# Kernel optimization log

Hardware: AMD Instinct MI355X
Metric: run time of the kernel (lower is better)

## Reference

```python
import jax, jax.numpy as jnp
import numpy as np

B, F_DIM, FH, FW = 2, 2048, 64, 128
C, H, W = 19, 512, 1024


def resize_bilinear_ac(x, h, w):
    # align_corners=True bilinear resize of (B, C, H, W) -> (B, C, h, w)
    Bx, Cx, Hx, Wx = x.shape
    ys = jnp.linspace(0.0, Hx - 1.0, h)
    xs = jnp.linspace(0.0, Wx - 1.0, w)
    y0 = jnp.floor(ys).astype(jnp.int32)
    y1 = jnp.minimum(y0 + 1, Hx - 1)
    wy = (ys - y0).astype(x.dtype)
    x0 = jnp.floor(xs).astype(jnp.int32)
    x1 = jnp.minimum(x0 + 1, Wx - 1)
    wx = (xs - x0).astype(x.dtype)
    r = x[:, :, y0, :] * (1 - wy)[None, None, :, None] + x[:, :, y1, :] * wy[None, None, :, None]
    return r[:, :, :, x0] * (1 - wx) + r[:, :, :, x1] * wx


def setup_inputs() -> dict:
    key = jax.random.key(0)
    k1, k2, k3, k4 = jax.random.split(key, 4)
    return {
        "source_feat": jax.random.normal(k1, (B, F_DIM, FH, FW), dtype=jnp.float32),
        "source_softmax": jax.random.uniform(k2, (B, C, H, W), dtype=jnp.float32),
        "target_feat": jax.random.normal(k3, (B, F_DIM, FH, FW), dtype=jnp.float32),
        "target_softmax": jax.random.uniform(k4, (B, C, H, W), dtype=jnp.float32),
        "norm_order": 2,
    }


def _process(feat, softmax):
    # feat: (B, F, h, w) -> (B*h*w, F); labels from bilinear-downsampled softmax argmax
    h, w = feat.shape[2], feat.shape[3]
    f2 = feat.transpose(0, 2, 3, 1).reshape(-1, feat.shape[1])
    sm_dws = resize_bilinear_ac(softmax, h, w)
    labels = jnp.argmax(sm_dws, axis=1).reshape(-1)
    return f2, labels


def _forward(source_feat, source_softmax, target_feat, target_softmax, p):
    num_class = source_softmax.shape[1]
    fdim = source_feat.shape[1]
    sf, sl = _process(source_feat, source_softmax)
    tf, tl = _process(target_feat, target_softmax)

    # mixed centroids: per-class mean over concatenated source+target pixels
    sum_s = jax.ops.segment_sum(sf, sl, num_segments=num_class)
    cnt_s = jax.ops.segment_sum(jnp.ones(sf.shape[0], sf.dtype), sl, num_segments=num_class)
    sum_t = jax.ops.segment_sum(tf, tl, num_segments=num_class)
    cnt_t = jax.ops.segment_sum(jnp.ones(tf.shape[0], tf.dtype), tl, num_segments=num_class)
    cnt = cnt_s + cnt_t
    seen = cnt > 0
    centroids = (sum_s + sum_t) / jnp.maximum(cnt, 1.0)[:, None]  # (C, F)

    inv_p = 1.0 / p

    def f_dist(f2, lab, cnt_d):
        # torch: sum_i norm(centroid_i - feat_i, p) / (n_i * F) over classes with n_i>0, / count
        dp = jnp.sum(jnp.abs(f2 - centroids[lab]) ** p, axis=1)  # (N,)
        ssq = jax.ops.segment_sum(dp, lab, num_segments=num_class)  # (C,)
        valid = cnt_d > 0
        ssq_safe = jnp.where(valid, ssq, 1.0)
        per = ssq_safe ** inv_p / (jnp.maximum(cnt_d, 1.0) * fdim)
        return jnp.sum(jnp.where(valid, per, 0.0)) / jnp.sum(valid).astype(f2.dtype)

    f_dist_source = f_dist(sf, sl, cnt_s)
    f_dist_target = f_dist(tf, tl, cnt_t)

    # intra-domain centroid-to-centroid distance over seen classes
    n_seen = jnp.sum(seen).astype(centroids.dtype)
    diffp = jnp.sum(jnp.abs(centroids[:, None, :] - centroids[None, :, :]) ** p, axis=-1)  # (C, C)
    pair_mask = seen[:, None] & seen[None, :] & (~jnp.eye(num_class, dtype=bool))
    row = jnp.sum(jnp.where(pair_mask, diffp, 0.0), axis=1)
    row_safe = jnp.where(seen, row, 1.0)
    per_i = row_safe ** inv_p / ((n_seen - 1.0) * fdim)
    c_dist = jnp.sum(jnp.where(seen, per_i, 0.0)) / n_seen

    return jnp.stack([c_dist, f_dist_source, f_dist_target])


def reference(source_feat, source_softmax, target_feat, target_softmax, norm_order):
    return _forward(source_feat, source_softmax, target_feat, target_softmax, norm_order)
```

## Files before the change

### kernel.cpp

```cpp
#include <hip/hip_runtime.h>
#include <hip/hip_bf16.h>

#define BB 2
#define FDIM 2048
#define FH 64
#define FW 128
#define NPIX (FH*FW)
#define NC 19
#define SH 512
#define SW 1024

#define KS 4
#define PXS (NPIX/KS)

#define OFF_GCNT  0
#define OFF_SQP   38912
#define OFF_SUMP  194560
#define OFF_LAB   2684928
#define OFF_CENT  2717696
#define OFF_DOTSP 2873344
#define OFF_PQP   2875168
#define OFF_CNTF  2876384
#define OFF_ROW   2876536

typedef __attribute__((ext_vector_type(8))) short short8v;
typedef __attribute__((ext_vector_type(4))) float f32x4;
typedef __attribute__((ext_vector_type(4))) float f4v;

__device__ inline short f32_to_bf16_bits(float x) {
  __hip_bfloat16 h = __float2bfloat16(x);
  return *reinterpret_cast<short*>(&h);
}
__device__ inline float bf16_bits_to_f32(short s) {
  unsigned u = ((unsigned)s & 0xFFFFu) << 16;
  return __uint_as_float(u);
}

__global__ __launch_bounds__(256) void labels_kernel(
    const float* __restrict__ sm_s, const float* __restrict__ sm_t,
    unsigned char* __restrict__ labels, unsigned int* __restrict__ gcnt) {
  __shared__ unsigned int lcnt[NC];
  int tid = threadIdx.x;
  if (tid < NC) lcnt[tid] = 0u;
  __syncthreads();

  int g = blockIdx.x * 256 + tid;
  int pixid = g >> 2;
  int sub = g & 3;
  int dom = pixid >> 14;
  int rem = pixid & 16383;
  int b   = rem >> 13;
  int pix = rem & (NPIX - 1);
  int oy  = pix >> 7;
  int ox  = pix & (FW - 1);

  const float* sm = dom ? sm_t : sm_s;

  const float step_y = 511.0f / 63.0f;
  const float step_x = 1023.0f / 127.0f;
  float fy = __fmul_rn((float)oy, step_y);
  float fx = __fmul_rn((float)ox, step_x);
  int y0 = (int)floorf(fy); int y1 = min(y0 + 1, SH - 1);
  int x0 = (int)floorf(fx); int x1 = min(x0 + 1, SW - 1);
  float wy = __fsub_rn(fy, (float)y0);
  float wx = __fsub_rn(fx, (float)x0);
  float omwy = __fsub_rn(1.0f, wy);
  float omwx = __fsub_rn(1.0f, wx);

  const float* base = sm + (size_t)b * (NC * SH * SW);
  float best = -1.0f; int bestc = 127;
  for (int c = sub; c < NC; c += 4) {
    const float* p = base + (size_t)c * (SH * SW);
    float v00 = p[y0 * SW + x0];
    float v01 = p[y0 * SW + x1];
    float v10 = p[y1 * SW + x0];
    float v11 = p[y1 * SW + x1];
    float r0  = __fadd_rn(__fmul_rn(v00, omwy), __fmul_rn(v10, wy));
    float r1  = __fadd_rn(__fmul_rn(v01, omwy), __fmul_rn(v11, wy));
    float val = __fadd_rn(__fmul_rn(r0, omwx), __fmul_rn(r1, wx));
    if (val > best) { best = val; bestc = c; }
  }
#pragma unroll
  for (int off = 1; off <= 2; off <<= 1) {
    float ov = __shfl_xor(best, off, 64);
    int   oc = __shfl_xor(bestc, off, 64);
    if (ov > best || (ov == best && oc < bestc)) { best = ov; bestc = oc; }
  }
  if (sub == 0) {
    labels[pixid] = (unsigned char)bestc;
    atomicAdd(&lcnt[bestc], 1u);
  }
  __syncthreads();
  if (tid < NC) gcnt[blockIdx.x * NC + tid] = lcnt[tid];
}

__global__ __launch_bounds__(256, 8) void segsum_kernel(
    const float* __restrict__ feat_s, const float* __restrict__ feat_t,
    const unsigned char* __restrict__ labels,
    float* __restrict__ sump, float* __restrict__ sq_p) {
  __shared__ unsigned short Abuf[4][2][16][64];

  int tid = threadIdx.x;
  int wv = tid >> 6, l = tid & 63;
  int m16 = l & 15, grp = l >> 4;
  int lrow = l >> 4;
  int lpx  = (l & 15) * 4;

  int low = blockIdx.x & 255;
  int hi  = blockIdx.x >> 8;
  int d = low >> 7, strip = low & 127;
  int b = hi & 1, ks = hi >> 1;

  const float* feat = d ? feat_t : feat_s;
  int px0 = ks * PXS + wv * 512;
  const float* fbase = feat + ((size_t)(b * FDIM + strip * 16)) * NPIX + px0;
  const unsigned char* labp = labels + (d * 2 + b) * NPIX + px0;

  unsigned short (*mybuf)[16][64] = Abuf[wv];

  f32x4 accS0 = {0.f,0.f,0.f,0.f}, accS1 = {0.f,0.f,0.f,0.f};
  f32x4 accQ0 = {0.f,0.f,0.f,0.f}, accQ1 = {0.f,0.f,0.f,0.f};

  f4v ld0[4], ld1[4];

#define LOADW(REG, W)                                                         \
  _Pragma("unroll") for (int r = 0; r < 4; ++r)                               \
    REG[r] = __builtin_nontemporal_load(                                      \
        (const f4v*)(fbase + (size_t)(r * 4 + lrow) * NPIX + (W) * 64 + lpx));

#define WRITEW(REG, CUR)                                                      \
  _Pragma("unroll") for (int r = 0; r < 4; ++r) {                             \
    int row = r * 4 + lrow;                                                   \
    unsigned u0 = ((unsigned)(unsigned short)f32_to_bf16_bits(REG[r].x)) |    \
                  (((unsigned)(unsigned short)f32_to_bf16_bits(REG[r].y)) << 16);\
    unsigned u1 = ((unsigned)(unsigned short)f32_to_bf16_bits(REG[r].z)) |    \
                  (((unsigned)(unsigned short)f32_to_bf16_bits(REG[r].w)) << 16);\
    int wbyte = (row * 128 + lpx * 2) ^ ((row & 7) << 4);                     \
    *(uint2*)((char*)&mybuf[CUR][0][0] + wbyte) = make_uint2(u0, u1);         \
  }

#define COMPW(W, CUR)                                                         \
  _Pragma("unroll") for (int t = 0; t < 2; ++t) {                             \
    int rbyte = (m16 * 128 + t * 64 + grp * 16) ^ ((m16 & 7) << 4);           \
    short8v a = *(const short8v*)((const char*)&mybuf[CUR][0][0] + rbyte);    \
    short8v a2;                                                               \
    _Pragma("unroll") for (int j = 0; j < 8; ++j) {                           \
      float x = bf16_bits_to_f32(a[j]);                                       \
      a2[j] = f32_to_bf16_bits(x * x);                                        \
    }                                                                         \
    uint2 lw = *(const uint2*)(labp + (W) * 64 + t * 32 + grp * 8);           \
    short8v b0, b1;                                                           \
    _Pragma("unroll") for (int j = 0; j < 8; ++j) {                           \
      unsigned lab = ((j < 4 ? lw.x : lw.y) >> ((j & 3) * 8)) & 0xFFu;        \
      b0[j] = (lab == (unsigned)m16)        ? (short)0x3F80 : (short)0;       \
      b1[j] = (lab == (unsigned)(m16 + 16)) ? (short)0x3F80 : (short)0;       \
    }                                                                         \
    accS0 = __builtin_amdgcn_mfma_f32_16x16x32_bf16(a,  b0, accS0, 0, 0, 0);  \
    accS1 = __builtin_amdgcn_mfma_f32_16x16x32_bf16(a,  b1, accS1, 0, 0, 0);  \
    accQ0 = __builtin_amdgcn_mfma_f32_16x16x32_bf16(a2, b0, accQ0, 0, 0, 0);  \
    accQ1 = __builtin_amdgcn_mfma_f32_16x16x32_bf16(a2, b1, accQ1, 0, 0, 0);  \
  }

  LOADW(ld0, 0);
  WRITEW(ld0, 0);
  LOADW(ld0, 1);

#pragma unroll
  for (int w = 0; w < 8; w += 2) {
    if (w + 2 < 8) { LOADW(ld1, w + 2); }
    COMPW(w, 0);
    if (w + 1 < 8) { WRITEW(ld0, 1); }
    if (w + 3 < 8) { LOADW(ld0, w + 3); }
    COMPW(w + 1, 1);
    if (w + 2 < 8) { WRITEW(ld1, 0); }
  }
#undef LOADW
#undef WRITEW
#undef COMPW

  __syncthreads();
  float* Sred = (float*)&Abuf[0][0][0][0];
  float* Qred = Sred + 4 * 19 * 16;

  int c0 = l & 15, frb = (l >> 4) * 4;
  *(f32x4*)&Sred[(wv * 19 + c0) * 16 + frb] = accS0;
  if (c0 < 3) *(f32x4*)&Sred[(wv * 19 + 16 + c0) * 16 + frb] = accS1;

  float q0 = accQ0[0] + accQ0[1] + accQ0[2] + accQ0[3];
  float q1 = accQ1[0] + accQ1[1] + accQ1[2] + accQ1[3];
  q0 += __shfl_xor(q0, 16, 64); q0 += __shfl_xor(q0, 32, 64);
  q1 += __shfl_xor(q1, 16, 64); q1 += __shfl_xor(q1, 32, 64);
  if (l < 16) Qred[wv * 19 + l] = q0;
  if (l < 3)  Qred[wv * 19 + 16 + l] = q1;
  __syncthreads();

  float* myslice = sump + ((size_t)(hi * 2 + d) * NC) * FDIM + strip * 16;
  for (int t = tid; t < NC * 16; t += 256) {
    int c = t >> 4, fr = t & 15;
    float sv = Sred[(0 * 19 + c) * 16 + fr] + Sred[(1 * 19 + c) * 16 + fr] +
               Sred[(2 * 19 + c) * 16 + fr] + Sred[(3 * 19 + c) * 16 + fr];
    myslice[(size_t)c * FDIM + fr] = sv;
  }
  if (tid < NC) {
    float qv = Qred[tid] + Qred[19 + tid] + Qred[38 + tid] + Qred[57 + tid];
    sq_p[(size_t)((hi * 2 + d) * 128 + strip) * NC + tid] = qv;
  }
}

__device__ inline float block_reduce(float v, float* red, int tid) {
  red[tid] = v; __syncthreads();
  for (int s = 128; s > 0; s >>= 1) {
    if (tid < s) red[tid] += red[tid + s];
    __syncthreads();
  }
  float r = red[0];
  __syncthreads();
  return r;
}

__global__ __launch_bounds__(256) void centroid_kernel(
    const float* __restrict__ sump, const float* __restrict__ sq_p,
    const unsigned int* __restrict__ gcnt,
    float* __restrict__ cent, float* __restrict__ dotsp,
    float* __restrict__ pqp, float* __restrict__ cntf) {
  __shared__ float red[256];
  int bid = blockIdx.x;
  int c = bid % NC, j = bid / NC;
  int tid = threadIdx.x;

  float cs = block_reduce((float)gcnt[tid * NC + c], red, tid);
  float ct = block_reduce((float)gcnt[(256 + tid) * NC + c], red, tid);
  if (tid == 0 && j == 0) { cntf[c] = cs; cntf[NC + c] = ct; }
  float denom = fmaxf(cs + ct, 1.0f);

  int f = j * 256 + tid;
  float ssv = 0.f, stv = 0.f;
#pragma unroll
  for (int hi = 0; hi < 8; ++hi) {
    ssv += sump[((size_t)(hi * 2 + 0) * NC + c) * FDIM + f];
    stv += sump[((size_t)(hi * 2 + 1) * NC + c) * FDIM + f];
  }
  float cf = (ssv + stv) / denom;
  cent[(size_t)c * FDIM + f] = cf;

  float rds = block_reduce(cf * ssv, red, tid);
  float rdt = block_reduce(cf * stv, red, tid);
  float rcc = block_reduce(cf * cf, red, tid);

  int slice = tid >> 4, strip = j * 16 + (tid & 15);
  float v = sq_p[(size_t)(slice * 128 + strip) * NC + c];
  float qs = block_reduce((slice & 1) == 0 ? v : 0.f, red, tid);
  float qt = block_reduce((slice & 1) == 1 ? v : 0.f, red, tid);

  if (tid == 0) {
    dotsp[(j * NC + c) * 3 + 0] = rds;
    dotsp[(j * NC + c) * 3 + 1] = rdt;
    dotsp[(j * NC + c) * 3 + 2] = rcc;
    pqp[(j * NC + c) * 2 + 0] = qs;
    pqp[(j * NC + c) * 2 + 1] = qt;
  }
}

__global__ __launch_bounds__(256) void pair_kernel(
    const float* __restrict__ cent, const float* __restrict__ cntf,
    float* __restrict__ row) {
  __shared__ float red[256];
  int i = blockIdx.x;
  int tid = threadIdx.x;
  bool seen_i = (cntf[i] + cntf[NC + i]) > 0.f;
  float acc = 0.f;
  if (seen_i) {
    for (int j = 0; j < NC; ++j) {
      if (j == i) continue;
      if ((cntf[j] + cntf[NC + j]) <= 0.f) continue;
      for (int f = tid; f < FDIM; f += 256) {
        float dd = cent[(size_t)i * FDIM + f] - cent[(size_t)j * FDIM + f];
        acc += dd * dd;
      }
    }
  }
  float r = block_reduce(acc, red, tid);
  if (tid == 0) row[i] = r;
}

__global__ void final_kernel(
    const float* __restrict__ cntf, const float* __restrict__ dotsp,
    const float* __restrict__ pqp, const float* __restrict__ row,
    float* __restrict__ out) {
  int l = threadIdx.x;
  const float fdim = (float)FDIM;
  bool isC = l < NC;
  int c = isC ? l : 0;

  float cs = 0.f, ct = 0.f, qs = 0.f, qt = 0.f;
  float d_s = 0.f, d_t = 0.f, cc = 0.f, rw = 0.f;
  if (isC) {
    cs = cntf[c]; ct = cntf[NC + c];
#pragma unroll
    for (int j = 0; j < 8; ++j) {
      qs  += pqp[(j * NC + c) * 2 + 0];
      qt  += pqp[(j * NC + c) * 2 + 1];
      d_s += dotsp[(j * NC + c) * 3 + 0];
      d_t += dotsp[(j * NC + c) * 3 + 1];
      cc  += dotsp[(j * NC + c) * 3 + 2];
    }
    rw = row[c];
  }
  bool seen = isC && (cs + ct > 0.f);
  float nseenf = (float)__popcll(__ballot(seen));
  float nvs    = (float)__popcll(__ballot(isC && cs > 0.f));
  float nvt    = (float)__popcll(__ballot(isC && ct > 0.f));

  float fs = 0.f, ft = 0.f, cd = 0.f;
  if (isC && cs > 0.f) {
    float ssq = fmaxf(qs - 2.0f * d_s + cs * cc, 0.f);
    fs = sqrtf(ssq) / (cs * fdim);
  }
  if (isC && ct > 0.f) {
    float ssq = fmaxf(qt - 2.0f * d_t + ct * cc, 0.f);
    ft = sqrtf(ssq) / (ct * fdim);
  }
  if (seen) cd = sqrtf(rw) / ((nseenf - 1.0f) * fdim);

#pragma unroll
  for (int off = 32; off > 0; off >>= 1) {
    fs += __shfl_down(fs, off, 64);
    ft += __shfl_down(ft, off, 64);
    cd += __shfl_down(cd, off, 64);
  }
  if (l == 0) {
    out[0] = cd / nseenf;
    out[1] = fs / nvs;
    out[2] = ft / nvt;
  }
}

extern "C" void kernel_launch(void* const* d_in, const int* in_sizes, int n_in,
                              void* d_out, int out_size, void* d_ws, size_t ws_size,
                              hipStream_t stream) {
  const float* sfeat = (const float*)d_in[0];
  const float* ssm   = (const float*)d_in[1];
  const float* tfeat = (const float*)d_in[2];
  const float* tsm   = (const float*)d_in[3];
  float* out = (float*)d_out;

  char* ws = (char*)d_ws;
  unsigned int*  gcnt   = (unsigned int*)(ws + OFF_GCNT);
  float*         sq_p   = (float*)(ws + OFF_SQP);
  float*         sump   = (float*)(ws + OFF_SUMP);
  unsigned char* labels = (unsigned char*)(ws + OFF_LAB);
  float*         cent   = (float*)(ws + OFF_CENT);
  float*         dotsp  = (float*)(ws + OFF_DOTSP);
  float*         pqp    = (float*)(ws + OFF_PQP);
  float*         cntf   = (float*)(ws + OFF_CNTF);
  float*         row    = (float*)(ws + OFF_ROW);

  labels_kernel  <<<512,    256, 0, stream>>>(ssm, tsm, labels, gcnt);
  segsum_kernel  <<<2048,   256, 0, stream>>>(sfeat, tfeat, labels, sump, sq_p);
  centroid_kernel<<<NC * 8, 256, 0, stream>>>(sump, sq_p, gcnt, cent, dotsp, pqp, cntf);
  pair_kernel    <<<NC,     256, 0, stream>>>(cent, cntf, row);
  final_kernel   <<<1,      64,  0, stream>>>(cntf, dotsp, pqp, row, out);
}
```

Measured before the change: 123.0 us.

## Use 8 lanes per pixel for labels and wider single-buffered segsum windows

The labels kernel now assigns 8 lanes per pixel instead of 4, doubling the block count and widening the shuffle argmax. This adds memory-level parallelism to the scattered softmax gathers. The segsum kernel drops LDS double buffering and processes 128-pixel windows with 8 loads in flight per lane, with occupancy lowered to 5 blocks. The centroid kernel and workspace offsets are adjusted to the doubled number of count partials. The risk is less load/compute overlap inside segsum, since it now has a single LDS buffer.

```diff
diff --git a/kernel.cpp b/kernel.cpp
--- a/kernel.cpp
+++ b/kernel.cpp
@@ -14,14 +14,14 @@
 #define PXS (NPIX/KS)
 
 #define OFF_GCNT  0
-#define OFF_SQP   38912
-#define OFF_SUMP  194560
-#define OFF_LAB   2684928
-#define OFF_CENT  2717696
-#define OFF_DOTSP 2873344
-#define OFF_PQP   2875168
-#define OFF_CNTF  2876384
-#define OFF_ROW   2876536
+#define OFF_SQP   77824
+#define OFF_SUMP  233472
+#define OFF_LAB   2723840
+#define OFF_CENT  2756608
+#define OFF_DOTSP 2912256
+#define OFF_PQP   2914080
+#define OFF_CNTF  2915296
+#define OFF_ROW   2915448
 
 typedef __attribute__((ext_vector_type(8))) short short8v;
 typedef __attribute__((ext_vector_type(4))) float f32x4;
@@ -45,8 +45,8 @@
   __syncthreads();
 
   int g = blockIdx.x * 256 + tid;
-  int pixid = g >> 2;
-  int sub = g & 3;
+  int pixid = g >> 3;
+  int sub = g & 7;
   int dom = pixid >> 14;
   int rem = pixid & 16383;
   int b   = rem >> 13;
@@ -69,7 +69,7 @@
 
   const float* base = sm + (size_t)b * (NC * SH * SW);
   float best = -1.0f; int bestc = 127;
-  for (int c = sub; c < NC; c += 4) {
+  for (int c = sub; c < NC; c += 8) {
     const float* p = base + (size_t)c * (SH * SW);
     float v00 = p[y0 * SW + x0];
     float v01 = p[y0 * SW + x1];
@@ -81,7 +81,7 @@
     if (val > best) { best = val; bestc = c; }
   }
 #pragma unroll
-  for (int off = 1; off <= 2; off <<= 1) {
+  for (int off = 1; off <= 4; off <<= 1) {
     float ov = __shfl_xor(best, off, 64);
     int   oc = __shfl_xor(bestc, off, 64);
     if (ov > best || (ov == best && oc < bestc)) { best = ov; bestc = oc; }
@@ -94,17 +94,17 @@
   if (tid < NC) gcnt[blockIdx.x * NC + tid] = lcnt[tid];
 }
 
-__global__ __launch_bounds__(256, 8) void segsum_kernel(
+__global__ __launch_bounds__(256, 5) void segsum_kernel(
     const float* __restrict__ feat_s, const float* __restrict__ feat_t,
     const unsigned char* __restrict__ labels,
     float* __restrict__ sump, float* __restrict__ sq_p) {
-  __shared__ unsigned short Abuf[4][2][16][64];
+  __shared__ unsigned short Abuf[4][16][128];
 
   int tid = threadIdx.x;
   int wv = tid >> 6, l = tid & 63;
   int m16 = l & 15, grp = l >> 4;
-  int lrow = l >> 4;
-  int lpx  = (l & 15) * 4;
+  int lhalf = l >> 5;
+  int lpx   = (l & 31) * 4;
 
   int low = blockIdx.x & 255;
   int hi  = blockIdx.x >> 8;
@@ -116,39 +116,39 @@
   const float* fbase = feat + ((size_t)(b * FDIM + strip * 16)) * NPIX + px0;
   const unsigned char* labp = labels + (d * 2 + b) * NPIX + px0;
 
-  unsigned short (*mybuf)[16][64] = Abuf[wv];
+  unsigned short (*mybuf)[128] = Abuf[wv];
 
   f32x4 accS0 = {0.f,0.f,0.f,0.f}, accS1 = {0.f,0.f,0.f,0.f};
   f32x4 accQ0 = {0.f,0.f,0.f,0.f}, accQ1 = {0.f,0.f,0.f,0.f};
 
-  f4v ld0[4], ld1[4];
-
-#define LOADW(REG, W)                                                         \
-  _Pragma("unroll") for (int r = 0; r < 4; ++r)                               \
-    REG[r] = __builtin_nontemporal_load(                                      \
-        (const f4v*)(fbase + (size_t)(r * 4 + lrow) * NPIX + (W) * 64 + lpx));
-
-#define WRITEW(REG, CUR)                                                      \
-  _Pragma("unroll") for (int r = 0; r < 4; ++r) {                             \
-    int row = r * 4 + lrow;                                                   \
-    unsigned u0 = ((unsigned)(unsigned short)f32_to_bf16_bits(REG[r].x)) |    \
-                  (((unsigned)(unsigned short)f32_to_bf16_bits(REG[r].y)) << 16);\
-    unsigned u1 = ((unsigned)(unsigned short)f32_to_bf16_bits(REG[r].z)) |    \
-                  (((unsigned)(unsigned short)f32_to_bf16_bits(REG[r].w)) << 16);\
-    int wbyte = (row * 128 + lpx * 2) ^ ((row & 7) << 4);                     \
-    *(uint2*)((char*)&mybuf[CUR][0][0] + wbyte) = make_uint2(u0, u1);         \
-  }
-
-#define COMPW(W, CUR)                                                         \
-  _Pragma("unroll") for (int t = 0; t < 2; ++t) {                             \
-    int rbyte = (m16 * 128 + t * 64 + grp * 16) ^ ((m16 & 7) << 4);           \
-    short8v a = *(const short8v*)((const char*)&mybuf[CUR][0][0] + rbyte);    \
+  f4v ld[8];
+
+#define LOADW(W)                                                              \
+  _Pragma("unroll") for (int r = 0; r < 8; ++r)                               \
+    ld[r] = __builtin_nontemporal_load(                                       \
+        (const f4v*)(fbase + (size_t)(r * 2 + lhalf) * NPIX + (W) * 128 + lpx));
+
+#define WRITEW()                                                              \
+  _Pragma("unroll") for (int r = 0; r < 8; ++r) {                             \
+    int row = r * 2 + lhalf;                                                  \
+    unsigned u0 = ((unsigned)(unsigned short)f32_to_bf16_bits(ld[r].x)) |     \
+                  (((unsigned)(unsigned short)f32_to_bf16_bits(ld[r].y)) << 16);\
+    unsigned u1 = ((unsigned)(unsigned short)f32_to_bf16_bits(ld[r].z)) |     \
+                  (((unsigned)(unsigned short)f32_to_bf16_bits(ld[r].w)) << 16);\
+    int wbyte = (row * 256 + (l & 31) * 8) ^ ((row & 7) << 4);                \
+    *(uint2*)((char*)&mybuf[0][0] + wbyte) = make_uint2(u0, u1);              \
+  }
+
+#define COMPW(W)                                                              \
+  _Pragma("unroll") for (int kt = 0; kt < 4; ++kt) {                          \
+    int rbyte = (m16 * 256 + kt * 64 + grp * 16) ^ ((m16 & 7) << 4);          \
+    short8v a = *(const short8v*)((const char*)&mybuf[0][0] + rbyte);         \
     short8v a2;                                                               \
     _Pragma("unroll") for (int j = 0; j < 8; ++j) {                           \
       float x = bf16_bits_to_f32(a[j]);                                       \
       a2[j] = f32_to_bf16_bits(x * x);                                        \
     }                                                                         \
-    uint2 lw = *(const uint2*)(labp + (W) * 64 + t * 32 + grp * 8);           \
+    uint2 lw = *(const uint2*)(labp + (W) * 128 + kt * 32 + grp * 8);         \
     short8v b0, b1;                                                           \
     _Pragma("unroll") for (int j = 0; j < 8; ++j) {                           \
       unsigned lab = ((j < 4 ? lw.x : lw.y) >> ((j & 3) * 8)) & 0xFFu;        \
@@ -161,25 +161,21 @@
     accQ1 = __builtin_amdgcn_mfma_f32_16x16x32_bf16(a2, b1, accQ1, 0, 0, 0);  \
   }
 
-  LOADW(ld0, 0);
-  WRITEW(ld0, 0);
-  LOADW(ld0, 1);
-
-#pragma unroll
-  for (int w = 0; w < 8; w += 2) {
-    if (w + 2 < 8) { LOADW(ld1, w + 2); }
-    COMPW(w, 0);
-    if (w + 1 < 8) { WRITEW(ld0, 1); }
-    if (w + 3 < 8) { LOADW(ld0, w + 3); }
-    COMPW(w + 1, 1);
-    if (w + 2 < 8) { WRITEW(ld1, 0); }
+  LOADW(0);
+  WRITEW();
+
+#pragma unroll
+  for (int w = 0; w < 4; ++w) {
+    if (w < 3) { LOADW(w + 1); }
+    COMPW(w);
+    if (w < 3) { WRITEW(); }
   }
 #undef LOADW
 #undef WRITEW
 #undef COMPW
 
   __syncthreads();
-  float* Sred = (float*)&Abuf[0][0][0][0];
+  float* Sred = (float*)&Abuf[0][0][0];
   float* Qred = Sred + 4 * 19 * 16;
 
   int c0 = l & 15, frb = (l >> 4) * 4;
@@ -228,8 +224,10 @@
   int c = bid % NC, j = bid / NC;
   int tid = threadIdx.x;
 
-  float cs = block_reduce((float)gcnt[tid * NC + c], red, tid);
-  float ct = block_reduce((float)gcnt[(256 + tid) * NC + c], red, tid);
+  float csp = (float)gcnt[tid * NC + c] + (float)gcnt[(256 + tid) * NC + c];
+  float ctp = (float)gcnt[(512 + tid) * NC + c] + (float)gcnt[(768 + tid) * NC + c];
+  float cs = block_reduce(csp, red, tid);
+  float ct = block_reduce(ctp, red, tid);
   if (tid == 0 && j == 0) { cntf[c] = cs; cntf[NC + c] = ct; }
   float denom = fmaxf(cs + ct, 1.0f);
 
@@ -355,7 +353,7 @@
   float*         cntf   = (float*)(ws + OFF_CNTF);
   float*         row    = (float*)(ws + OFF_ROW);
 
-  labels_kernel  <<<512,    256, 0, stream>>>(ssm, tsm, labels, gcnt);
+  labels_kernel  <<<1024,   256, 0, stream>>>(ssm, tsm, labels, gcnt);
   segsum_kernel  <<<2048,   256, 0, stream>>>(sfeat, tfeat, labels, sump, sq_p);
   centroid_kernel<<<NC * 8, 256, 0, stream>>>(sump, sq_p, gcnt, cent, dotsp, pqp, cntf);
   pair_kernel    <<<NC,     256, 0, stream>>>(cent, cntf, row);
```

Result: faster. 106.8 us (median of 2 runs) (-13.1%).
